# Optimization experiments

Measured on AMD Instinct MI355X. Metric: run time of the kernel, lower is better.

The kernel has to match this reference:

```python
import jax, jax.numpy as jnp
import numpy as np

P, R, S = 512, 128, 128   # num_proposal, ref_length, src_length
K = 3                      # top-k per row/column
THRESHOLD = 0.05
MUTUAL = False
CONDITIONAL = True


def setup_inputs() -> dict:
    key = jax.random.key(0)
    k1, k2, k3, k4 = jax.random.split(key, 4)
    return {
        "matching_score_map": jax.random.normal(k1, (P, R, S), dtype=jnp.float32),
        "ref_knn_masks": jax.random.bernoulli(k2, 0.9, (P, R)),
        "src_knn_masks": jax.random.bernoulli(k3, 0.9, (P, S)),
        "node_corr_scores": jax.random.uniform(k4, (P,), dtype=jnp.float32),
    }


def reference(matching_score_map, ref_knn_masks, src_knn_masks, node_corr_scores):
    # matching_score_map: [P, R, S] log-scores -> exp, as in torch forward
    m = jnp.exp(matching_score_map)
    p, r, s = m.shape
    # corr_mask_map = ref_mask[:, :, None] & src_mask[:, None, :] -> [P, R, S]
    corr_mask_map = jnp.logical_and(ref_knn_masks[:, :, None], src_knn_masks[:, None, :])

    pidx = jnp.arange(p)[:, None, None]

    # top-k along src dim (dim=2), scatter back into a sparse score map
    ref_topk_scores, ref_topk_idx = jax.lax.top_k(m, K)           # [P, R, K]
    ridx = jnp.arange(r)[None, :, None]
    ref_score_map = jnp.zeros_like(m).at[pidx, ridx, ref_topk_idx].set(ref_topk_scores)

    # top-k along ref dim (dim=1): transpose, top_k, scatter, transpose back
    mt = jnp.swapaxes(m, 1, 2)                                    # [P, S, R]
    src_topk_scores, src_topk_idx = jax.lax.top_k(mt, K)          # [P, S, K]
    sidx = jnp.arange(s)[None, :, None]
    src_score_map = jnp.swapaxes(
        jnp.zeros_like(mt).at[pidx, sidx, src_topk_idx].set(src_topk_scores), 1, 2
    )

    ref_corr_map = jnp.logical_and(ref_score_map > THRESHOLD, corr_mask_map)
    src_corr_map = jnp.logical_and(src_score_map > THRESHOLD, corr_mask_map)

    score_map = (ref_score_map + src_score_map) * 0.5
    if MUTUAL:
        corr_map = jnp.logical_and(ref_corr_map, src_corr_map)
    else:
        corr_map = jnp.logical_or(ref_corr_map, src_corr_map)
    if CONDITIONAL:
        score_map = score_map * node_corr_scores[:, None, None]
    return score_map, corr_map
```

## Files before the change

kernel.cpp:

```cpp
#include <hip/hip_runtime.h>


constexpr int NP = 512;
constexpr int NR = 128;
constexpr int NS = 128;
constexpr int RS = NR * NS;
constexpr float THRESHOLD = 0.05f;
constexpr float NEG_INF = -3.4e38f;

__device__ __forceinline__ void top3_insert(float v, float& m0, float& m1, float& m2) {
    bool g2 = v > m2, g1 = v > m1, g0 = v > m0;
    float n2 = g1 ? m1 : (g2 ? v : m2);
    float n1 = g0 ? m0 : (g1 ? v : m1);
    float n0 = g0 ? v : m0;
    m0 = n0; m1 = n1; m2 = n2;
}

__device__ __forceinline__ void shfl_merge3(int d, float& m0, float& m1, float& m2) {
    float o0 = __shfl_xor(m0, d);
    float o1 = __shfl_xor(m1, d);
    float o2 = __shfl_xor(m2, d);
    top3_insert(o0, m0, m1, m2);
    top3_insert(o1, m0, m1, m2);
    top3_insert(o2, m0, m1, m2);
}

__global__ __launch_bounds__(512, 4) void fused_kernel(
    const float* __restrict__ in,
    const int*   __restrict__ rmask,
    const int*   __restrict__ smask,
    const float* __restrict__ ncs,
    float*       __restrict__ ws,
    float*       __restrict__ out)
{
    __shared__ float4 tile4[RS / 4];
    const int p   = blockIdx.x;
    const int t   = threadIdx.x;
    const int row = t >> 2;
    const int q   = t & 3;

    const float4* b4 = (const float4*)(in + (size_t)p * RS);
    float* ws_col = ws + (size_t)p * 128;

    float r0 = NEG_INF, r1 = NEG_INF, r2 = NEG_INF;
    #pragma unroll
    for (int j = 0; j < 8; ++j) {
        int c4 = q + 4 * j;
        float4 v = b4[row * 32 + c4];
        tile4[row * 32 + (c4 ^ (row & 31))] = v;
        top3_insert(v.x, r0, r1, r2);
        top3_insert(v.y, r0, r1, r2);
        top3_insert(v.z, r0, r1, r2);
        top3_insert(v.w, r0, r1, r2);
    }
    shfl_merge3(1, r0, r1, r2);
    shfl_merge3(2, r0, r1, r2);
    const float tr = r2;
    __syncthreads();

    {
        const int col = t >> 2, seg = t & 3;
        const int c4c = col >> 2, cw = col & 3;
        const float* tf = (const float*)tile4;
        float c0 = NEG_INF, c1 = NEG_INF, c2 = NEG_INF;
        #pragma unroll 8
        for (int i = 0; i < 32; ++i) {
            int r = 4 * seg + (i & 3) + 16 * (i >> 2);
            float v = tf[r * 128 + ((c4c ^ (r & 31)) << 2) + cw];
            top3_insert(v, c0, c1, c2);
        }
        shfl_merge3(1, c0, c1, c2);
        shfl_merge3(2, c0, c1, c2);
        if (seg == 0) ws_col[col] = c2;
    }
    __threadfence_block();
    __syncthreads();

    const float nc = ncs[p];
    const bool  mr = rmask[p * NR + row] != 0;
    float4* sc4 = (float4*)(out + (size_t)p * RS);
    float4* co4 = (float4*)(out + (size_t)(NP + p) * RS);
    const float4* wc4 = (const float4*)ws_col;
    const int4*   sm4 = (const int4*)(smask + (size_t)p * NS);

    #pragma unroll
    for (int j = 0; j < 8; ++j) {
        int c4 = q + 4 * j;
        float4 x  = tile4[row * 32 + (c4 ^ (row & 31))];
        float4 tc = wc4[c4];
        int4   ms = sm4[c4];
        float4 sc, co;

        {   float m  = __expf(x.x);
            float rs = (x.x >= tr)   ? m : 0.f;
            float cs = (x.x >= tc.x) ? m : 0.f;
            sc.x = 0.5f * (rs + cs) * nc;
            co.x = (mr && (ms.x != 0) && (rs > THRESHOLD || cs > THRESHOLD)) ? 1.f : 0.f; }
        {   float m  = __expf(x.y);
            float rs = (x.y >= tr)   ? m : 0.f;
            float cs = (x.y >= tc.y) ? m : 0.f;
            sc.y = 0.5f * (rs + cs) * nc;
            co.y = (mr && (ms.y != 0) && (rs > THRESHOLD || cs > THRESHOLD)) ? 1.f : 0.f; }
        {   float m  = __expf(x.z);
            float rs = (x.z >= tr)   ? m : 0.f;
            float cs = (x.z >= tc.z) ? m : 0.f;
            sc.z = 0.5f * (rs + cs) * nc;
            co.z = (mr && (ms.z != 0) && (rs > THRESHOLD || cs > THRESHOLD)) ? 1.f : 0.f; }
        {   float m  = __expf(x.w);
            float rs = (x.w >= tr)   ? m : 0.f;
            float cs = (x.w >= tc.w) ? m : 0.f;
            sc.w = 0.5f * (rs + cs) * nc;
            co.w = (mr && (ms.w != 0) && (rs > THRESHOLD || cs > THRESHOLD)) ? 1.f : 0.f; }

        sc4[row * 32 + c4] = sc;
        co4[row * 32 + c4] = co;
    }
}

extern "C" void kernel_launch(void* const* d_in, const int* in_sizes, int n_in,
                              void* d_out, int out_size, void* d_ws, size_t ws_size,
                              hipStream_t stream) {
    const float* msm   = (const float*)d_in[0];
    const int*   rmask = (const int*)  d_in[1];
    const int*   smask = (const int*)  d_in[2];
    const float* ncs   = (const float*)d_in[3];
    float* out = (float*)d_out;
    float* ws  = (float*)d_ws;

    fused_kernel<<<NP, 512, 0, stream>>>(msm, rmask, smask, ncs, ws, out);
}
```

Measured before the change: 98.13 us.

## Use med3 top-3, keep tile in registers, LDS column thresholds, nontemporal IO

Replaces the branchy top-3 insertion with fmed3/fmax instructions. Keeps the loaded values in registers for the final pass instead of rereading LDS. Column thresholds move from a global workspace into shared memory, which needs an extra barrier. Loads and stores become nontemporal, and the score and correspondence math is simplified. The aim is to cut ALU work, global round trips and cache pollution, at the cost of more register pressure from holding 32 floats per thread.

```diff
diff --git a/kernel.cpp b/kernel.cpp
--- a/kernel.cpp
+++ b/kernel.cpp
@@ -1,5 +1,8 @@
 #include <hip/hip_runtime.h>
 
+
+typedef float  vf4 __attribute__((ext_vector_type(4)));
+typedef int    vi4 __attribute__((ext_vector_type(4)));
 
 constexpr int NP = 512;
 constexpr int NR = 128;
@@ -9,11 +12,10 @@
 constexpr float NEG_INF = -3.4e38f;
 
 __device__ __forceinline__ void top3_insert(float v, float& m0, float& m1, float& m2) {
-    bool g2 = v > m2, g1 = v > m1, g0 = v > m0;
-    float n2 = g1 ? m1 : (g2 ? v : m2);
-    float n1 = g0 ? m0 : (g1 ? v : m1);
-    float n0 = g0 ? v : m0;
-    m0 = n0; m1 = n1; m2 = n2;
+    float n1 = __builtin_amdgcn_fmed3f(v, m0, m1);
+    float n2 = __builtin_amdgcn_fmed3f(v, m1, m2);
+    m0 = fmaxf(m0, v);
+    m1 = n1; m2 = n2;
 }
 
 __device__ __forceinline__ void shfl_merge3(int d, float& m0, float& m1, float& m2) {
@@ -30,34 +32,34 @@
     const int*   __restrict__ rmask,
     const int*   __restrict__ smask,
     const float* __restrict__ ncs,
-    float*       __restrict__ ws,
     float*       __restrict__ out)
 {
-    __shared__ float4 tile4[RS / 4];
+    __shared__ vf4 tile4[RS / 4];
     const int p   = blockIdx.x;
     const int t   = threadIdx.x;
     const int row = t >> 2;
     const int q   = t & 3;
 
-    const float4* b4 = (const float4*)(in + (size_t)p * RS);
-    float* ws_col = ws + (size_t)p * 128;
+    const vf4* b4 = (const vf4*)(in + (size_t)p * RS);
 
+    vf4 x[8];
     float r0 = NEG_INF, r1 = NEG_INF, r2 = NEG_INF;
     #pragma unroll
     for (int j = 0; j < 8; ++j) {
         int c4 = q + 4 * j;
-        float4 v = b4[row * 32 + c4];
-        tile4[row * 32 + (c4 ^ (row & 31))] = v;
-        top3_insert(v.x, r0, r1, r2);
-        top3_insert(v.y, r0, r1, r2);
-        top3_insert(v.z, r0, r1, r2);
-        top3_insert(v.w, r0, r1, r2);
+        x[j] = __builtin_nontemporal_load(&b4[row * 32 + c4]);
+        tile4[row * 32 + (c4 ^ (row & 31))] = x[j];
+        top3_insert(x[j].x, r0, r1, r2);
+        top3_insert(x[j].y, r0, r1, r2);
+        top3_insert(x[j].z, r0, r1, r2);
+        top3_insert(x[j].w, r0, r1, r2);
     }
     shfl_merge3(1, r0, r1, r2);
     shfl_merge3(2, r0, r1, r2);
     const float tr = r2;
     __syncthreads();
 
+    float c2_third;
     {
         const int col = t >> 2, seg = t & 3;
         const int c4c = col >> 2, cw = col & 3;
@@ -66,54 +68,57 @@
         #pragma unroll 8
         for (int i = 0; i < 32; ++i) {
             int r = 4 * seg + (i & 3) + 16 * (i >> 2);
-            float v = tf[r * 128 + ((c4c ^ (r & 31)) << 2) + cw];
-            top3_insert(v, c0, c1, c2);
+            top3_insert(tf[r * 128 + ((c4c ^ (r & 31)) << 2) + cw], c0, c1, c2);
         }
         shfl_merge3(1, c0, c1, c2);
         shfl_merge3(2, c0, c1, c2);
-        if (seg == 0) ws_col[col] = c2;
+        c2_third = c2;
     }
-    __threadfence_block();
+    __syncthreads();
+    {
+        float* thirds = (float*)tile4;
+        if ((t & 3) == 0) thirds[t >> 2] = c2_third;
+    }
     __syncthreads();
 
-    const float nc = ncs[p];
-    const bool  mr = rmask[p * NR + row] != 0;
-    float4* sc4 = (float4*)(out + (size_t)p * RS);
-    float4* co4 = (float4*)(out + (size_t)(NP + p) * RS);
-    const float4* wc4 = (const float4*)ws_col;
-    const int4*   sm4 = (const int4*)(smask + (size_t)p * NS);
+    const float* thirds = (const float*)tile4;
+    const float halfnc = 0.5f * ncs[p];
+    const float mrf    = (rmask[p * NR + row] != 0) ? 1.0f : 0.0f;
+    vf4* sc4 = (vf4*)(out + (size_t)p * RS);
+    vf4* co4 = (vf4*)(out + (size_t)(NP + p) * RS);
+    const vi4* sm4 = (const vi4*)(smask + (size_t)p * NS);
 
     #pragma unroll
     for (int j = 0; j < 8; ++j) {
         int c4 = q + 4 * j;
-        float4 x  = tile4[row * 32 + (c4 ^ (row & 31))];
-        float4 tc = wc4[c4];
-        int4   ms = sm4[c4];
-        float4 sc, co;
+        vf4 tc = ((const vf4*)thirds)[c4];
+        vi4 ms = __builtin_nontemporal_load(&sm4[c4]);
+        vf4 v  = x[j];
+        vf4 sc, co;
 
-        {   float m  = __expf(x.x);
-            float rs = (x.x >= tr)   ? m : 0.f;
-            float cs = (x.x >= tc.x) ? m : 0.f;
-            sc.x = 0.5f * (rs + cs) * nc;
-            co.x = (mr && (ms.x != 0) && (rs > THRESHOLD || cs > THRESHOLD)) ? 1.f : 0.f; }
-        {   float m  = __expf(x.y);
-            float rs = (x.y >= tr)   ? m : 0.f;
-            float cs = (x.y >= tc.y) ? m : 0.f;
-            sc.y = 0.5f * (rs + cs) * nc;
-            co.y = (mr && (ms.y != 0) && (rs > THRESHOLD || cs > THRESHOLD)) ? 1.f : 0.f; }
-        {   float m  = __expf(x.z);
-            float rs = (x.z >= tr)   ? m : 0.f;
-            float cs = (x.z >= tc.z) ? m : 0.f;
-            sc.z = 0.5f * (rs + cs) * nc;
-            co.z = (mr && (ms.z != 0) && (rs > THRESHOLD || cs > THRESHOLD)) ? 1.f : 0.f; }
-        {   float m  = __expf(x.w);
-            float rs = (x.w >= tr)   ? m : 0.f;
-            float cs = (x.w >= tc.w) ? m : 0.f;
-            sc.w = 0.5f * (rs + cs) * nc;
-            co.w = (mr && (ms.w != 0) && (rs > THRESHOLD || cs > THRESHOLD)) ? 1.f : 0.f; }
+        {   float e = __expf(v.x);
+            float w = ((v.x >= tr) ? halfnc : 0.f) + ((v.x >= tc.x) ? halfnc : 0.f);
+            sc.x = e * w;
+            float mk = (ms.x != 0) ? mrf : 0.f;
+            co.x = (e > THRESHOLD && w > 0.f) ? mk : 0.f; }
+        {   float e = __expf(v.y);
+            float w = ((v.y >= tr) ? halfnc : 0.f) + ((v.y >= tc.y) ? halfnc : 0.f);
+            sc.y = e * w;
+            float mk = (ms.y != 0) ? mrf : 0.f;
+            co.y = (e > THRESHOLD && w > 0.f) ? mk : 0.f; }
+        {   float e = __expf(v.z);
+            float w = ((v.z >= tr) ? halfnc : 0.f) + ((v.z >= tc.z) ? halfnc : 0.f);
+            sc.z = e * w;
+            float mk = (ms.z != 0) ? mrf : 0.f;
+            co.z = (e > THRESHOLD && w > 0.f) ? mk : 0.f; }
+        {   float e = __expf(v.w);
+            float w = ((v.w >= tr) ? halfnc : 0.f) + ((v.w >= tc.w) ? halfnc : 0.f);
+            sc.w = e * w;
+            float mk = (ms.w != 0) ? mrf : 0.f;
+            co.w = (e > THRESHOLD && w > 0.f) ? mk : 0.f; }
 
-        sc4[row * 32 + c4] = sc;
-        co4[row * 32 + c4] = co;
+        __builtin_nontemporal_store(sc, &sc4[row * 32 + c4]);
+        __builtin_nontemporal_store(co, &co4[row * 32 + c4]);
     }
 }
 
@@ -125,7 +130,6 @@
     const int*   smask = (const int*)  d_in[2];
     const float* ncs   = (const float*)d_in[3];
     float* out = (float*)d_out;
-    float* ws  = (float*)d_ws;
 
-    fused_kernel<<<NP, 512, 0, stream>>>(msm, rmask, smask, ncs, ws, out);
+    fused_kernel<<<NP, 512, 0, stream>>>(msm, rmask, smask, ncs, out);
 }
```

New measurement: 107.4 us. 1.09x slower.
